# Performance work log

Hardware: AMD Instinct MI355X
Metric: run time of the kernel (lower is better)

Reference implementation:

```python
import jax, jax.numpy as jnp
import numpy as np


def conv2d(x, w, b=None, pad=0):
    out = jax.lax.conv_general_dilated(
        x, w, window_strides=(1, 1), padding=[(pad, pad), (pad, pad)],
        dimension_numbers=('NCHW', 'OIHW', 'NCHW'))
    if b is not None:
        out = out + b[None, :, None, None]
    return out


def maxpool2(x):
    return jax.lax.reduce_window(x, -jnp.inf, jax.lax.max,
                                 (1, 1, 2, 2), (1, 1, 2, 2), 'VALID')


def conv_offset_2d(x, offset_w):
    """ConvOffset2D: learn per-pixel (dy,dx) offsets via a 3x3 conv (C->2C, no
    bias), then bilinearly resample x at grid+offset. Faithful to the repo,
    including its raw (B,2C,H,W)->(B*C,H,W,2) memory reinterpretation."""
    B, C, H, W = x.shape
    off = conv2d(x, offset_w, pad=1)                  # (B, 2C, H, W)
    off = off.reshape(B * C, H, W, 2)                 # raw row-major reshape (as in repo)
    xf = x.reshape(B * C, H, W)
    gy, gx = jnp.meshgrid(jnp.arange(H, dtype=x.dtype),
                          jnp.arange(W, dtype=x.dtype), indexing='ij')
    coords = off + jnp.stack([gy, gx], axis=-1)       # (BC, H, W, 2) = (y, x)
    cy = jnp.clip(coords[..., 0], 0.0, float(H - 1))
    cx = jnp.clip(coords[..., 1], 0.0, float(W - 1))
    y0 = jnp.floor(cy)
    x0 = jnp.floor(cx)
    y0i = y0.astype(jnp.int32)
    x0i = x0.astype(jnp.int32)
    y1i = jnp.ceil(cy).astype(jnp.int32)
    x1i = jnp.ceil(cx).astype(jnp.int32)
    bidx = jnp.arange(B * C)[:, None, None]
    v_lt = xf[bidx, y0i, x0i]
    v_rt = xf[bidx, y0i, x1i]
    v_lb = xf[bidx, y1i, x0i]
    v_rb = xf[bidx, y1i, x1i]
    tx = cx - x0
    ty = cy - y0
    v_t = v_lt + (v_rt - v_lt) * tx
    v_b = v_lb + (v_rb - v_lb) * tx
    out = v_t + (v_b - v_t) * ty
    return out.reshape(B, C, H, W)


def setup_inputs() -> dict:
    key = jax.random.key(0)
    ks = jax.random.split(key, 9)
    B = 2048
    inp = {
        'x': jax.random.normal(ks[0], (B, 1, 28, 28), dtype=jnp.float32),
        'off1_w': jax.random.normal(ks[1], (2, 1, 3, 3), dtype=jnp.float32) * 0.01,
        'conv1_w': jax.random.normal(ks[2], (16, 1, 5, 5), dtype=jnp.float32) * 0.1,
        'conv1_b': jax.random.normal(ks[3], (16,), dtype=jnp.float32) * 0.01,
        'off2_w': jax.random.normal(ks[4], (32, 16, 3, 3), dtype=jnp.float32) * 0.01,
        'conv2_w': jax.random.normal(ks[5], (32, 16, 5, 5), dtype=jnp.float32) * 0.05,
        'conv2_b': jax.random.normal(ks[6], (32,), dtype=jnp.float32) * 0.01,
        'fc_w': jax.random.normal(ks[7], (10, 32 * 7 * 7), dtype=jnp.float32) * 0.02,
        'fc_b': jax.random.normal(ks[8], (10,), dtype=jnp.float32) * 0.01,
    }
    return inp


def reference(x, off1_w, conv1_w, conv1_b, off2_w, conv2_w, conv2_b, fc_w, fc_b):
    # block 1: deform sample -> 5x5 conv pad 2 -> relu -> maxpool 2
    h = conv_offset_2d(x, off1_w)
    h = maxpool2(jax.nn.relu(conv2d(h, conv1_w, conv1_b, pad=2)))   # (B,16,14,14)
    # block 2
    h = conv_offset_2d(h, off2_w)
    h = maxpool2(jax.nn.relu(conv2d(h, conv2_w, conv2_b, pad=2)))   # (B,32,7,7)
    # classifier
    flat = h.reshape(h.shape[0], -1)                                # (B, 1568)
    return flat @ fc_w.T + fc_b
```

## Files before the change

### kernel.cpp

```cpp
#include <hip/hip_runtime.h>
#include <hip/hip_bf16.h>


#define B_IMG 2048

typedef short bf16x8 __attribute__((ext_vector_type(8)));
typedef float f32x4 __attribute__((ext_vector_type(4)));

__global__ __launch_bounds__(256) void k_prep(const float* __restrict__ w_off2,
                                              const float* __restrict__ w_c2,
                                              const float* __restrict__ w_c1,
                                              __hip_bfloat16* __restrict__ wqo,
                                              __hip_bfloat16* __restrict__ wq2,
                                              __hip_bfloat16* __restrict__ wqc1) {
    int e = blockIdx.x * 256 + threadIdx.x;
    if (e < 5120) {
        int sp = e >> 10, rem = e & 1023, oc = rem >> 5, k = rem & 31;
        int sl = k >> 4, ic = k & 15, s = 2 * sp + sl;
        wqo[e] = __float2bfloat16(s < 9 ? w_off2[(oc * 16 + ic) * 9 + s] : 0.f);
    } else if (e < 18432) {
        int e2 = e - 5120;
        int sp = e2 >> 10, rem = e2 & 1023, oc = rem >> 5, k = rem & 31;
        int sl = k >> 4, ic = k & 15, s = 2 * sp + sl;
        wq2[e2] = __float2bfloat16(s < 25 ? w_c2[(oc * 16 + ic) * 25 + s] : 0.f);
    } else if (e < 18944) {
        int e3 = e - 18432;
        int oc = e3 >> 5, k = e3 & 31;
        wqc1[e3] = __float2bfloat16(k < 25 ? w_c1[oc * 25 + k] : 0.f);
    }
}

__global__ __launch_bounds__(256, 4) void k_net(const float* __restrict__ x,
                                                const float* __restrict__ off1_w,
                                                const __hip_bfloat16* __restrict__ wqc1,
                                                const float* __restrict__ conv1_b,
                                                const __hip_bfloat16* __restrict__ wqo,
                                                const __hip_bfloat16* __restrict__ wq2,
                                                const float* __restrict__ conv2_b,
                                                const float* __restrict__ fc_w,
                                                const float* __restrict__ fc_b,
                                                float* __restrict__ out) {
    __shared__ __align__(16) char s5[12544];
    __shared__ __align__(16) __hip_bfloat16 imgb[16 * 16 * 16];
    __shared__ __align__(16) __hip_bfloat16 img2b[18 * 20 * 16];

    float* xs = (float*)s5;
    __hip_bfloat16* img2bf = (__hip_bfloat16*)(s5 + 3600);
    _Float16* offbuf = (_Float16*)s5;
    float* pl    = (float*)s5;
    float* wredp = (float*)(s5 + 6272);

    int b = blockIdx.x, t = threadIdx.x;

    float xreg[4];
#pragma unroll
    for (int j = 0; j < 4; ++j) {
        int i = t + j * 256;
        xreg[j] = (i < 784) ? x[b * 784 + i] : 0.f;
    }
    for (int i = t; i < 900; i += 256) xs[i] = 0.f;
    for (int i = t; i < 576; i += 256) ((unsigned int*)img2bf)[i] = 0u;
    for (int i = t; i < 480; i += 256) {
        int word = i & 7;
        int cell = i >> 3;
        int row, col;
        if (cell < 16) { row = 0; col = cell; }
        else if (cell < 32) { row = 15; col = cell - 16; }
        else { int q = cell - 32; row = 1 + (q >> 1); col = (q & 1) * 15; }
        ((unsigned int*)imgb)[(row * 16 + col) * 8 + word] = 0u;
    }
    for (int p = t; p < 360; p += 256) {
        int r = p / 20, cc = p % 20;
        if (r < 2 || r > 15 || cc < 2 || cc > 15) {
            unsigned int* dst = (unsigned int*)&img2b[p * 16];
#pragma unroll
            for (int q = 0; q < 8; ++q) dst[q] = 0u;
        }
    }
    __syncthreads();
#pragma unroll
    for (int j = 0; j < 4; ++j) {
        int i = t + j * 256;
        if (i < 784) xs[(i / 28 + 1) * 30 + (i % 28) + 1] = xreg[j];
    }
    __syncthreads();

    {
        int h = t / 28, w = t % 28;
        for (int p = t; p < 784; p += 256) {
            int c = (h >= 14) ? 1 : 0;
            int hp = h - 14 * c;
            const float* wo = off1_w + c * 9;
            float off[2];
#pragma unroll
            for (int k = 0; k < 2; ++k) {
                int e = 2 * w + k;
                int wrap = (e >= 28) ? 1 : 0;
                int hh = 2 * hp + wrap;
                int ww = e - 28 * wrap;
                float s = 0.f;
#pragma unroll
                for (int dy = 0; dy < 3; ++dy)
#pragma unroll
                    for (int dx = 0; dx < 3; ++dx)
                        s += wo[dy * 3 + dx] * xs[(hh + dy) * 30 + ww + dx];
                off[k] = s;
            }
            float cy = fminf(fmaxf((float)h + off[0], 0.f), 27.f);
            float cx = fminf(fmaxf((float)w + off[1], 0.f), 27.f);
            float y0f = floorf(cy), x0f = floorf(cx);
            int y0 = (int)y0f, x0 = (int)x0f;
            int y1 = (int)ceilf(cy), x1 = (int)ceilf(cx);
            float ty = cy - y0f, tx = cx - x0f;
            float vlt = xs[(y0 + 1) * 30 + x0 + 1], vrt = xs[(y0 + 1) * 30 + x1 + 1];
            float vlb = xs[(y1 + 1) * 30 + x0 + 1], vrb = xs[(y1 + 1) * 30 + x1 + 1];
            float vt = vlt + (vrt - vlt) * tx;
            float vb = vlb + (vrb - vlb) * tx;
            img2bf[(h + 2) * 36 + (w + 2)] = __float2bfloat16(vt + (vb - vt) * ty);
            h += 9; w += 4;
            if (w >= 28) { w -= 28; h += 1; }
        }
    }
    __syncthreads();

    int wv_ = t >> 6, li = t & 63;
    int lx = li & 15, lg = li >> 4;

    {
        const bf16x8* wc1v = (const bf16x8*)wqc1;
        bf16x8 af1 = wc1v[lx * 4 + lg];
        float b4[4];
#pragma unroll
        for (int r = 0; r < 4; ++r) b4[r] = conv1_b[lg * 4 + r];
        int toff[8];
#pragma unroll
        for (int j = 0; j < 8; ++j) {
            int tt = 8 * lg + j;
            int dyq = tt / 5, dxq = tt - 5 * dyq;
            toff[j] = (tt < 25) ? (dyq * 36 + dxq) : 0;
        }
        int ypstart = (wv_ < 2) ? wv_ * 4 : 8 + (wv_ - 2) * 3;
        int ypcnt = (wv_ < 2) ? 4 : 3;
        const unsigned short* ib28 = (const unsigned short*)img2bf;
        for (int u = 0; u < 4; ++u) {
            if (u < ypcnt) {
                int yp = ypstart + u;
#pragma unroll
                for (int xh = 0; xh < 2; ++xh) {
                    int xp = xh * 16 + lx;
                    f32x4 a0 = (f32x4){0.f, 0.f, 0.f, 0.f};
                    f32x4 a1 = (f32x4){0.f, 0.f, 0.f, 0.f};
#pragma unroll
                    for (int yy = 0; yy < 2; ++yy) {
                        int base16 = (2 * yp + yy) * 36 + xp;
                        unsigned short uu[8];
#pragma unroll
                        for (int j = 0; j < 8; ++j)
                            uu[j] = ib28[base16 + toff[j]];
                        bf16x8 bq = {(short)uu[0], (short)uu[1], (short)uu[2], (short)uu[3],
                                     (short)uu[4], (short)uu[5], (short)uu[6], (short)uu[7]};
                        if (yy == 0)
                            a0 = __builtin_amdgcn_mfma_f32_16x16x32_bf16(af1, bq, a0, 0, 0, 0);
                        else
                            a1 = __builtin_amdgcn_mfma_f32_16x16x32_bf16(af1, bq, a1, 0, 0, 0);
                    }
#pragma unroll
                    for (int r = 0; r < 4; ++r) {
                        float v = fmaxf(fmaxf(a0[r], a1[r]) + b4[r], 0.f);
                        float p = __shfl_xor(v, 1);
                        float m = fmaxf(v, p);
                        if (((xp & 1) == 0) && xp < 28) {
                            int oc = lg * 4 + r;
                            imgb[(yp + 1) * 256 + ((xp >> 1) + 1) * 16 + oc] = __float2bfloat16(m);
                        }
                    }
                }
            }
        }
    }
    __syncthreads();

    int och = wv_ & 1, yh = wv_ >> 1;
    int nrows = yh ? 6 : 8;
    int aidx = (och * 16 + lx) * 4 + lg;

    {
        const bf16x8* wA = (const bf16x8*)wqo;
        bf16x8 afc = wA[aidx];
        int slA = lg >> 1, icsel = lg & 1;
        f32x4 acc[8];
#pragma unroll
        for (int y = 0; y < 8; ++y) acc[y] = (f32x4){0.f, 0.f, 0.f, 0.f};
        const bf16x8* ib = (const bf16x8*)imgb;
        __builtin_amdgcn_s_setprio(1);
#pragma unroll
        for (int sp = 0; sp < 5; ++sp) {
            bf16x8 afn;
            if (sp < 4) afn = wA[(sp + 1) * 128 + aidx];
            int s0 = 2 * sp + slA;
            int dy = s0 / 3, dx = s0 % 3;
            if (s0 >= 9) { dy = 0; dx = 0; }
            int base = dy * 32 + (lx + dx) * 2 + icsel;
#pragma unroll
            for (int y = 0; y < 8; ++y) {
                if (y < nrows) {
                    bf16x8 bfr = ib[base + (yh * 8 + y) * 32];
                    acc[y] = __builtin_amdgcn_mfma_f32_16x16x32_bf16(afc, bfr, acc[y], 0, 0, 0);
                }
            }
            afc = afn;
        }
        __builtin_amdgcn_s_setprio(0);
        if (lx < 14) {
#pragma unroll
            for (int y = 0; y < 8; ++y) {
                if (y < nrows) {
                    int yy = yh * 8 + y;
#pragma unroll
                    for (int r = 0; r < 4; ++r) {
                        int oc = och * 16 + lg * 4 + r;
                        offbuf[oc * 196 + yy * 14 + lx] = (_Float16)acc[y][r];
                    }
                }
            }
        }
    }
    __syncthreads();

    {
        int c = t & 15;
        int rem0 = t >> 4;
        int h = (rem0 >= 14) ? 1 : 0;
        int w = rem0 - 14 * h;
#pragma unroll
        for (int u = 0; u < 13; ++u) {
            if (h < 14) {
                int pidx = c * 196 + h * 14 + w;
                unsigned int pr = ((const unsigned int*)offbuf)[pidx];
                unsigned short lo16 = (unsigned short)(pr & 0xFFFFu);
                unsigned short hi16 = (unsigned short)(pr >> 16);
                float offy = (float)(*(const _Float16*)&lo16);
                float offx = (float)(*(const _Float16*)&hi16);
                float cy = fminf(fmaxf((float)h + offy, 0.f), 13.f);
                float cx = fminf(fmaxf((float)w + offx, 0.f), 13.f);
                float y0f = floorf(cy), x0f = floorf(cx);
                int y0 = (int)y0f, x0 = (int)x0f;
                int y1 = (int)ceilf(cy), x1 = (int)ceilf(cx);
                float ty = cy - y0f, tx = cx - x0f;
                float vlt = __bfloat162float(imgb[(y0 + 1) * 256 + (x0 + 1) * 16 + c]);
                float vrt = __bfloat162float(imgb[(y0 + 1) * 256 + (x1 + 1) * 16 + c]);
                float vlb = __bfloat162float(imgb[(y1 + 1) * 256 + (x0 + 1) * 16 + c]);
                float vrb = __bfloat162float(imgb[(y1 + 1) * 256 + (x1 + 1) * 16 + c]);
                float vt = vlt + (vrt - vlt) * tx;
                float vb = vlb + (vrb - vlb) * tx;
                img2b[((h + 2) * 20 + (w + 2)) * 16 + c] = __float2bfloat16(vt + (vb - vt) * ty);
            }
            h += 1; w += 2;
            if (w >= 14) { w -= 14; h += 1; }
        }
    }
    __syncthreads();

    {
        const bf16x8* wB = (const bf16x8*)wq2;
        bf16x8 afc = wB[aidx];
        int sl = lg >> 1, icg = lg & 1;
        float bias_r[4];
#pragma unroll
        for (int r = 0; r < 4; ++r) bias_r[r] = conv2_b[och * 16 + lg * 4 + r];
        f32x4 acc[8];
#pragma unroll
        for (int y = 0; y < 8; ++y) acc[y] = (f32x4){0.f, 0.f, 0.f, 0.f};
        const bf16x8* ib2 = (const bf16x8*)img2b;
        __builtin_amdgcn_s_setprio(1);
#pragma unroll
        for (int sp = 0; sp < 13; ++sp) {
            bf16x8 afn;
            if (sp < 12) afn = wB[(sp + 1) * 128 + aidx];
            int s0 = 2 * sp + sl;
            int dy = s0 / 5, dx = s0 % 5;
            if (s0 >= 25) { dy = 0; dx = 0; }
            int base = (lx + dx) * 2 + icg;
#pragma unroll
            for (int y = 0; y < 8; ++y) {
                if (y < nrows) {
                    bf16x8 bfr = ib2[base + (yh * 8 + y + dy) * 40];
                    acc[y] = __builtin_amdgcn_mfma_f32_16x16x32_bf16(afc, bfr, acc[y], 0, 0, 0);
                }
            }
            afc = afn;
        }
        __builtin_amdgcn_s_setprio(0);
        __syncthreads();
        int npool = yh ? 3 : 4;
#pragma unroll
        for (int u = 0; u < 4; ++u) {
            if (u < npool) {
                int i = yh * 4 + u;
#pragma unroll
                for (int r = 0; r < 4; ++r) {
                    int oc = och * 16 + lg * 4 + r;
                    float v = fmaxf(fmaxf(acc[2 * u][r], acc[2 * u + 1][r]) + bias_r[r], 0.f);
                    float p = __shfl_xor(v, 1);
                    float m = fmaxf(v, p);
                    if (((lx & 1) == 0) && lx < 14)
                        pl[oc * 49 + i * 7 + (lx >> 1)] = m;
                }
            }
        }
    }
    __syncthreads();

    float facc[10];
#pragma unroll
    for (int o = 0; o < 10; ++o) facc[o] = 0.f;
#pragma unroll
    for (int it = 0; it < 2; ++it) {
        int k = t * 4 + it * 1024;
        if (k < 1568) {
            float4 v = *(const float4*)&pl[k];
#pragma unroll
            for (int o = 0; o < 10; ++o) {
                float4 w4 = *(const float4*)&fc_w[o * 1568 + k];
                facc[o] += v.x * w4.x + v.y * w4.y + v.z * w4.z + v.w * w4.w;
            }
        }
    }
#pragma unroll
    for (int o = 0; o < 10; ++o) {
        float s = facc[o];
#pragma unroll
        for (int m = 32; m > 0; m >>= 1) s += __shfl_xor(s, m);
        if (li == 0) wredp[o * 4 + wv_] = s;
    }
    __syncthreads();
    if (t < 10)
        out[b * 10 + t] = fc_b[t] + wredp[t * 4] + wredp[t * 4 + 1] + wredp[t * 4 + 2] + wredp[t * 4 + 3];
}

extern "C" void kernel_launch(void* const* d_in, const int* in_sizes, int n_in,
                              void* d_out, int out_size, void* d_ws, size_t ws_size,
                              hipStream_t stream) {
    const float* x       = (const float*)d_in[0];
    const float* off1_w  = (const float*)d_in[1];
    const float* conv1_w = (const float*)d_in[2];
    const float* conv1_b = (const float*)d_in[3];
    const float* off2_w  = (const float*)d_in[4];
    const float* conv2_w = (const float*)d_in[5];
    const float* conv2_b = (const float*)d_in[6];
    const float* fc_w    = (const float*)d_in[7];
    const float* fc_b    = (const float*)d_in[8];
    float* out = (float*)d_out;

    char* ws = (char*)d_ws;
    __hip_bfloat16* wqo  = (__hip_bfloat16*)ws;
    __hip_bfloat16* wq2  = (__hip_bfloat16*)(ws + 10240);
    __hip_bfloat16* wqc1 = (__hip_bfloat16*)(ws + 36864);

    k_prep<<<74, 256, 0, stream>>>(off2_w, conv2_w, conv1_w, wqo, wq2, wqc1);
    k_net<<<B_IMG, 256, 0, stream>>>(x, off1_w, wqc1, conv1_b, wqo, wq2,
                                     conv2_b, fc_w, fc_b, out);
}
```

Baseline: 57.25 us.

## Process two images per 512-thread block and alias img2b onto scratch LDS

```diff
diff --git a/kernel.cpp b/kernel.cpp
--- a/kernel.cpp
+++ b/kernel.cpp
@@ -30,7 +30,7 @@
     }
 }
 
-__global__ __launch_bounds__(256, 4) void k_net(const float* __restrict__ x,
+__global__ __launch_bounds__(512, 2) void k_net(const float* __restrict__ x,
                                                 const float* __restrict__ off1_w,
                                                 const __hip_bfloat16* __restrict__ wqc1,
                                                 const float* __restrict__ conv1_b,
@@ -40,17 +40,22 @@
                                                 const float* __restrict__ fc_w,
                                                 const float* __restrict__ fc_b,
                                                 float* __restrict__ out) {
-    __shared__ __align__(16) char s5[12544];
-    __shared__ __align__(16) __hip_bfloat16 imgb[16 * 16 * 16];
-    __shared__ __align__(16) __hip_bfloat16 img2b[18 * 20 * 16];
-
-    float* xs = (float*)s5;
-    __hip_bfloat16* img2bf = (__hip_bfloat16*)(s5 + 3600);
-    _Float16* offbuf = (_Float16*)s5;
-    float* pl    = (float*)s5;
-    float* wredp = (float*)(s5 + 6272);
-
-    int b = blockIdx.x, t = threadIdx.x;
+    __shared__ __align__(16) char s5[2][12544];
+    __shared__ __align__(16) __hip_bfloat16 imgb[2][16 * 16 * 16];
+
+    int t0 = threadIdx.x;
+    int img = t0 >> 8;
+    int t = t0 & 255;
+    int b = blockIdx.x * 2 + img;
+
+    char* s5i = s5[img];
+    float* xs = (float*)s5i;
+    __hip_bfloat16* img2bf = (__hip_bfloat16*)(s5i + 3600);
+    _Float16* offbuf = (_Float16*)s5i;
+    __hip_bfloat16* img2b = (__hip_bfloat16*)s5i;
+    __hip_bfloat16* imgbI = imgb[img];
+    float* pl    = (float*)imgbI;
+    float* wredp = (float*)((char*)imgbI + 6272);
 
     float xreg[4];
 #pragma unroll
@@ -67,15 +72,7 @@
         if (cell < 16) { row = 0; col = cell; }
         else if (cell < 32) { row = 15; col = cell - 16; }
         else { int q = cell - 32; row = 1 + (q >> 1); col = (q & 1) * 15; }
-        ((unsigned int*)imgb)[(row * 16 + col) * 8 + word] = 0u;
-    }
-    for (int p = t; p < 360; p += 256) {
-        int r = p / 20, cc = p % 20;
-        if (r < 2 || r > 15 || cc < 2 || cc > 15) {
-            unsigned int* dst = (unsigned int*)&img2b[p * 16];
-#pragma unroll
-            for (int q = 0; q < 8; ++q) dst[q] = 0u;
-        }
+        ((unsigned int*)imgbI)[(row * 16 + col) * 8 + word] = 0u;
     }
     __syncthreads();
 #pragma unroll
@@ -171,7 +168,7 @@
                         float m = fmaxf(v, p);
                         if (((xp & 1) == 0) && xp < 28) {
                             int oc = lg * 4 + r;
-                            imgb[(yp + 1) * 256 + ((xp >> 1) + 1) * 16 + oc] = __float2bfloat16(m);
+                            imgbI[(yp + 1) * 256 + ((xp >> 1) + 1) * 16 + oc] = __float2bfloat16(m);
                         }
                     }
                 }
@@ -191,7 +188,7 @@
         f32x4 acc[8];
 #pragma unroll
         for (int y = 0; y < 8; ++y) acc[y] = (f32x4){0.f, 0.f, 0.f, 0.f};
-        const bf16x8* ib = (const bf16x8*)imgb;
+        const bf16x8* ib = (const bf16x8*)imgbI;
         __builtin_amdgcn_s_setprio(1);
 #pragma unroll
         for (int sp = 0; sp < 5; ++sp) {
@@ -228,35 +225,60 @@
     __syncthreads();
 
     {
-        int c = t & 15;
-        int rem0 = t >> 4;
-        int h = (rem0 >= 14) ? 1 : 0;
-        int w = rem0 - 14 * h;
-#pragma unroll
-        for (int u = 0; u < 13; ++u) {
-            if (h < 14) {
-                int pidx = c * 196 + h * 14 + w;
-                unsigned int pr = ((const unsigned int*)offbuf)[pidx];
-                unsigned short lo16 = (unsigned short)(pr & 0xFFFFu);
-                unsigned short hi16 = (unsigned short)(pr >> 16);
-                float offy = (float)(*(const _Float16*)&lo16);
-                float offx = (float)(*(const _Float16*)&hi16);
-                float cy = fminf(fmaxf((float)h + offy, 0.f), 13.f);
-                float cx = fminf(fmaxf((float)w + offx, 0.f), 13.f);
-                float y0f = floorf(cy), x0f = floorf(cx);
-                int y0 = (int)y0f, x0 = (int)x0f;
-                int y1 = (int)ceilf(cy), x1 = (int)ceilf(cx);
-                float ty = cy - y0f, tx = cx - x0f;
-                float vlt = __bfloat162float(imgb[(y0 + 1) * 256 + (x0 + 1) * 16 + c]);
-                float vrt = __bfloat162float(imgb[(y0 + 1) * 256 + (x1 + 1) * 16 + c]);
-                float vlb = __bfloat162float(imgb[(y1 + 1) * 256 + (x0 + 1) * 16 + c]);
-                float vrb = __bfloat162float(imgb[(y1 + 1) * 256 + (x1 + 1) * 16 + c]);
-                float vt = vlt + (vrt - vlt) * tx;
-                float vb = vlb + (vrb - vlb) * tx;
-                img2b[((h + 2) * 20 + (w + 2)) * 16 + c] = __float2bfloat16(vt + (vb - vt) * ty);
-            }
-            h += 1; w += 2;
-            if (w >= 14) { w -= 14; h += 1; }
+        float vres[13];
+        {
+            int c = t & 15;
+            int rem0 = t >> 4;
+            int h = (rem0 >= 14) ? 1 : 0;
+            int w = rem0 - 14 * h;
+#pragma unroll
+            for (int u = 0; u < 13; ++u) {
+                if (h < 14) {
+                    int pidx = c * 196 + h * 14 + w;
+                    unsigned int pr = ((const unsigned int*)offbuf)[pidx];
+                    unsigned short lo16 = (unsigned short)(pr & 0xFFFFu);
+                    unsigned short hi16 = (unsigned short)(pr >> 16);
+                    float offy = (float)(*(const _Float16*)&lo16);
+                    float offx = (float)(*(const _Float16*)&hi16);
+                    float cy = fminf(fmaxf((float)h + offy, 0.f), 13.f);
+                    float cx = fminf(fmaxf((float)w + offx, 0.f), 13.f);
+                    float y0f = floorf(cy), x0f = floorf(cx);
+                    int y0 = (int)y0f, x0 = (int)x0f;
+                    int y1 = (int)ceilf(cy), x1 = (int)ceilf(cx);
+                    float ty = cy - y0f, tx = cx - x0f;
+                    float vlt = __bfloat162float(imgbI[(y0 + 1) * 256 + (x0 + 1) * 16 + c]);
+                    float vrt = __bfloat162float(imgbI[(y0 + 1) * 256 + (x1 + 1) * 16 + c]);
+                    float vlb = __bfloat162float(imgbI[(y1 + 1) * 256 + (x0 + 1) * 16 + c]);
+                    float vrb = __bfloat162float(imgbI[(y1 + 1) * 256 + (x1 + 1) * 16 + c]);
+                    float vt = vlt + (vrt - vlt) * tx;
+                    float vb = vlb + (vrb - vlb) * tx;
+                    vres[u] = vt + (vb - vt) * ty;
+                }
+                h += 1; w += 2;
+                if (w >= 14) { w -= 14; h += 1; }
+            }
+        }
+        __syncthreads();
+        for (int p = t; p < 360; p += 256) {
+            int r = p / 20, cc = p % 20;
+            if (r < 2 || r > 15 || cc < 2 || cc > 15) {
+                unsigned int* dst = (unsigned int*)&img2b[p * 16];
+#pragma unroll
+                for (int q = 0; q < 8; ++q) dst[q] = 0u;
+            }
+        }
+        {
+            int c = t & 15;
+            int rem0 = t >> 4;
+            int h = (rem0 >= 14) ? 1 : 0;
+            int w = rem0 - 14 * h;
+#pragma unroll
+            for (int u = 0; u < 13; ++u) {
+                if (h < 14)
+                    img2b[((h + 2) * 20 + (w + 2)) * 16 + c] = __float2bfloat16(vres[u]);
+                h += 1; w += 2;
+                if (w >= 14) { w -= 14; h += 1; }
+            }
         }
     }
     __syncthreads();
@@ -291,7 +313,6 @@
             afc = afn;
         }
         __builtin_amdgcn_s_setprio(0);
-        __syncthreads();
         int npool = yh ? 3 : 4;
 #pragma unroll
         for (int u = 0; u < 4; ++u) {
@@ -358,6 +379,6 @@
     __hip_bfloat16* wqc1 = (__hip_bfloat16*)(ws + 36864);
 
     k_prep<<<74, 256, 0, stream>>>(off2_w, conv2_w, conv1_w, wqo, wq2, wqc1);
-    k_net<<<B_IMG, 256, 0, stream>>>(x, off1_w, wqc1, conv1_b, wqo, wq2,
-                                     conv2_b, fc_w, fc_b, out);
+    k_net<<<B_IMG / 2, 512, 0, stream>>>(x, off1_w, wqc1, conv1_b, wqo, wq2,
+                                         conv2_b, fc_w, fc_b, out);
 }
```

New measurement: 59.58 us. +4.1%, slower.
